# Optimization experiments

Hardware: AMD Instinct MI355X
Metric: run time of the kernel (lower is better)

Reference implementation:

```python
import jax, jax.numpy as jnp
import numpy as np
from jax import lax

B = 64
LATENT = 256
TARGET = LATENT // 2
ACT = 6
HID = 512
DSTATE = 16


def conv2d(x, w, b, stride=2):
    # torch Conv2d(k=4, stride=2, pad=1), w: (O,I,4,4)
    y = lax.conv_general_dilated(x, w, (stride, stride), ((1, 1), (1, 1)),
                                 dimension_numbers=('NCHW', 'OIHW', 'NCHW'))
    return y + b[None, :, None, None]


def deconv2d(x, w, b):
    # torch ConvTranspose2d(k=4, stride=2, pad=1), w: (I,O,4,4)
    w_ = jnp.flip(w, (2, 3)).transpose(1, 0, 2, 3)  # -> OIHW
    y = lax.conv_general_dilated(x, w_, (1, 1), ((2, 2), (2, 2)),
                                 lhs_dilation=(2, 2),
                                 dimension_numbers=('NCHW', 'OIHW', 'NCHW'))
    return y + b[None, :, None, None]


def linear(x, w, b=None):
    y = x @ w.T
    return y if b is None else y + b


def setup_inputs() -> dict:
    key = jax.random.key(0)
    ks = jax.random.split(key, 40)
    s = 0.02
    d = {
        'img_t': jax.random.normal(ks[0], (B, 3, 256, 256), jnp.float32),
        'action_prev': jax.random.normal(ks[1], (B, ACT), jnp.float32),
        'z_prev': jax.random.normal(ks[2], (B, LATENT), jnp.float32),
        'ssm_state_prev': jax.random.normal(ks[3], (B, HID, DSTATE), jnp.float32),
        'eps': jax.random.normal(ks[4], (B, LATENT), jnp.float32),
        # CNN encoder
        'conv1_w': jax.random.normal(ks[5], (32, 3, 4, 4)) * s, 'conv1_b': jnp.zeros(32),
        'conv2_w': jax.random.normal(ks[6], (64, 32, 4, 4)) * s, 'conv2_b': jnp.zeros(64),
        'conv3_w': jax.random.normal(ks[7], (128, 64, 4, 4)) * s, 'conv3_b': jnp.zeros(128),
        'conv4_w': jax.random.normal(ks[8], (256, 128, 4, 4)) * s, 'conv4_b': jnp.zeros(256),
        'enc_fc_w': jax.random.normal(ks[9], (512, 256 * 16 * 16)) * s, 'enc_fc_b': jnp.zeros(512),
        # heads
        'post_w': jax.random.normal(ks[10], (LATENT * 2, 512 + HID)) * s, 'post_b': jnp.zeros(LATENT * 2),
        'prior_w': jax.random.normal(ks[11], (LATENT * 2, HID)) * s, 'prior_b': jnp.zeros(LATENT * 2),
        # ssm input proj
        'ssm_in_w': jax.random.normal(ks[12], (HID, LATENT + ACT)) * s, 'ssm_in_b': jnp.zeros(HID),
        # selective SSM cell
        'A_log': jnp.log(jnp.tile(jnp.arange(1, DSTATE + 1, dtype=jnp.float32), (HID, 1))),
        'B_w': jax.random.normal(ks[13], (DSTATE, HID)) * s,
        'C_w': jax.random.normal(ks[14], (DSTATE, HID)) * s,
        'Delta_w': jax.random.normal(ks[15], (HID, HID)) * s, 'Delta_b': jnp.zeros(HID),
        'D': jnp.ones(HID),
        # mask decoder
        'dec_fc_w': jax.random.normal(ks[16], (128 * 16 * 16, TARGET)) * s, 'dec_fc_b': jnp.zeros(128 * 16 * 16),
        'dc1_w': jax.random.normal(ks[17], (128, 64, 4, 4)) * s, 'dc1_b': jnp.zeros(64),
        'dc2_w': jax.random.normal(ks[18], (64, 32, 4, 4)) * s, 'dc2_b': jnp.zeros(32),
        'dc3_w': jax.random.normal(ks[19], (32, 16, 4, 4)) * s, 'dc3_b': jnp.zeros(16),
        'dc4_w': jax.random.normal(ks[20], (16, 1, 4, 4)) * s, 'dc4_b': jnp.zeros(1),
    }
    return {k: v.astype(jnp.float32) for k, v in d.items()}


def reference(img_t, action_prev, z_prev, ssm_state_prev, eps,
              conv1_w, conv1_b, conv2_w, conv2_b, conv3_w, conv3_b, conv4_w, conv4_b,
              enc_fc_w, enc_fc_b, post_w, post_b, prior_w, prior_b,
              ssm_in_w, ssm_in_b, A_log, B_w, C_w, Delta_w, Delta_b, D,
              dec_fc_w, dec_fc_b, dc1_w, dc1_b, dc2_w, dc2_b, dc3_w, dc3_b, dc4_w, dc4_b):
    # SSM input projection + SiLU
    ssm_in = jax.nn.silu(linear(jnp.concatenate([z_prev, action_prev], -1), ssm_in_w, ssm_in_b))  # (B,HID)
    # Selective SSM cell (single step)
    A = -jnp.exp(A_log)                                   # (HID,DSTATE)
    B_t = linear(ssm_in, B_w)                              # (B,DSTATE)
    C_t = linear(ssm_in, C_w)                              # (B,DSTATE)
    Delta_t = jax.nn.softplus(linear(ssm_in, Delta_w, Delta_b))  # (B,HID)
    A_bar = jnp.exp(Delta_t[:, :, None] * A[None])        # (B,HID,DSTATE)
    Delta_B = Delta_t[:, :, None] * B_t[:, None, :]
    ssm_state_t = A_bar * ssm_state_prev + Delta_B * ssm_in[:, :, None]
    belief = jnp.sum(ssm_state_t * C_t[:, None, :], -1) + D * ssm_in  # (B,HID)
    # Prior
    mu_prior, logvar_prior = jnp.split(linear(belief, prior_w, prior_b), 2, axis=-1)
    # CNN encoder
    h = jax.nn.relu(conv2d(img_t, conv1_w, conv1_b))
    h = jax.nn.relu(conv2d(h, conv2_w, conv2_b))
    h = jax.nn.relu(conv2d(h, conv3_w, conv3_b))
    h = jax.nn.relu(conv2d(h, conv4_w, conv4_b))           # (B,256,16,16)
    cnn_feat = jax.nn.relu(linear(h.reshape(h.shape[0], -1), enc_fc_w, enc_fc_b))  # (B,512)
    # Posterior
    mu_post, logvar_post = jnp.split(linear(jnp.concatenate([cnn_feat, belief], -1), post_w, post_b), 2, axis=-1)
    z_t = mu_post + eps * jnp.exp(0.5 * logvar_post)
    # Mask decoder on target half of latent
    z_target = z_t[:, :TARGET]
    x = linear(z_target, dec_fc_w, dec_fc_b).reshape(-1, 128, 16, 16)
    x = jax.nn.relu(deconv2d(x, dc1_w, dc1_b))
    x = jax.nn.relu(deconv2d(x, dc2_w, dc2_b))
    x = jax.nn.relu(deconv2d(x, dc3_w, dc3_b))
    pred_mask_logits = deconv2d(x, dc4_w, dc4_b)           # (B,1,256,256)
    return (pred_mask_logits, z_t, ssm_state_t, mu_prior, logvar_prior, mu_post, logvar_post)
```

## Files before the change

kernel.cpp:

```cpp
#include <hip/hip_runtime.h>
#include <math.h>

#define BB 64
#define LATENT 256
#define ACTD 6
#define HIDD 512
#define DST 16

typedef __attribute__((ext_vector_type(8))) short bf16x8;
typedef __attribute__((ext_vector_type(4))) float f32x4;

static __device__ __forceinline__ ushort f2bf(float f) {
  unsigned u = __builtin_bit_cast(unsigned, f);
  unsigned r = (u + 0x7FFFu + ((u >> 16) & 1u)) >> 16;
  return (ushort)r;
}
static __device__ __forceinline__ float bf2f(ushort u) {
  return __builtin_bit_cast(float, ((unsigned)u) << 16);
}

#define O_PRED   0
#define O_ZT     4194304
#define O_STATE  4210688
#define O_MUP    4734976
#define O_LVP    4751360
#define O_MUPO   4767744
#define O_LVPO   4784128

#define W_BELIEF 67584u
#define W_CNN    100352u
#define W_ZB16   133120u
#define PW_C2    137216u
#define PW_C3    153600u
#define PW_C4    219136u
#define PW_D1    481280u
#define PW_D2    546816u
#define PW_D3    563200u
#define PW_C1    567296u
#define W_TIMG   602112u
#define W_H1B    13185024u
#define W_H2B    29962240u
#define W_H3B    38350848u
#define W_H4B    42545152u
#define W_SIWT   44642304u
#define W_DWT    44776448u
#define W_PRWT   45038592u
#define W_POWT   45300736u
#define W_ENCP   602112u
#define W_DECO   8990720u
#define W_D1O    10039296u
#define W_D2O    13185024u
#define W_D3O    17379328u

#define ENC_KS 128


static __device__ __forceinline__ void pack_conv_elem(const float* __restrict__ w,
                                                      ushort* __restrict__ o,
                                                      int Cout, int Cin, int id) {
  int NCH = Cin / 2;
  int per = NCH * 512;
  int mt = id / per, r = id % per;
  int kcg = r >> 9, s = r & 511;
  int kg = s >> 7, m = (s >> 3) & 15, k8 = s & 7;
  int co = mt * 16 + m;
  int k = kcg * 32 + kg * 8 + k8;
  int tap = k / Cin, ci = k % Cin;
  o[id] = f2bf(w[(size_t)(co * Cin + ci) * 16 + tap]);
}

static __device__ __forceinline__ void pack_deconv_elem(const float* __restrict__ w,
                                                        ushort* __restrict__ o,
                                                        int Cout, int Cin, int id) {
  int NCH = Cin / 8;
  int perM = NCH * 512;
  int perC = (Cout / 16) * perM;
  int cls = id / perC, r = id % perC;
  int mt = r / perM, r2 = r % perM;
  int kcg = r2 >> 9, s = r2 & 511;
  int kg = s >> 7, m = (s >> 3) & 15, k8 = s & 7;
  int co = mt * 16 + m;
  int k = kcg * 32 + kg * 8 + k8;
  int t = k / Cin, ci = k % Cin;
  int p = (cls >> 1) + 2 * (t >> 1);
  int q = (cls & 1) + 2 * (t & 1);
  o[id] = f2bf(w[(size_t)(ci * Cout + co) * 16 + p * 4 + q]);
}

static __device__ __forceinline__ void pack_conv1_elem(const float* __restrict__ w,
                                                       ushort* __restrict__ o, int id) {
  int mt = id >> 10, r = id & 1023;
  int kcg = r >> 9, s = r & 511;
  int kg = s >> 7, m = (s >> 3) & 15, k8 = s & 7;
  int co = mt * 16 + m;
  int k = kcg * 32 + kg * 8 + k8;
  int tap = k >> 2, ci = k & 3;
  o[id] = (ci < 3) ? f2bf(w[(size_t)(co * 3 + ci) * 16 + tap]) : (ushort)0;
}

__global__ __launch_bounds__(256) void k_pack_all(
    const float* __restrict__ c2w, const float* __restrict__ c3w,
    const float* __restrict__ c4w, const float* __restrict__ d1w,
    const float* __restrict__ d2w, const float* __restrict__ d3w,
    const float* __restrict__ c1w,
    const float* __restrict__ siw, const float* __restrict__ Dw,
    const float* __restrict__ prw, const float* __restrict__ pw,
    ushort* __restrict__ pc2, ushort* __restrict__ pc3, ushort* __restrict__ pc4,
    ushort* __restrict__ pd1, ushort* __restrict__ pd2, ushort* __restrict__ pd3,
    ushort* __restrict__ pc1,
    float* __restrict__ siwT, float* __restrict__ DwT,
    float* __restrict__ prwT, float* __restrict__ powT) {
  int id = blockIdx.x * 256 + threadIdx.x;
  if (id < 32768)            pack_conv_elem(c2w, pc2, 64, 32, id);
  else if (id < 163840)      pack_conv_elem(c3w, pc3, 128, 64, id - 32768);
  else if (id < 688128)      pack_conv_elem(c4w, pc4, 256, 128, id - 163840);
  else if (id < 819200)      pack_deconv_elem(d1w, pd1, 64, 128, id - 688128);
  else if (id < 851968)      pack_deconv_elem(d2w, pd2, 32, 64, id - 819200);
  else if (id < 860160)      pack_deconv_elem(d3w, pd3, 16, 32, id - 851968);
  else if (id < 862208)      pack_conv1_elem(c1w, pc1, id - 860160);
  else if (id < 996352) {
    int r = id - 862208; int k = r >> 9, h = r & 511;
    siwT[r] = siw[(size_t)h * (LATENT + ACTD) + k];
  } else if (id < 1258496) {
    int r = id - 996352; int k = r >> 9, h = r & 511;
    DwT[r] = Dw[(size_t)h * HIDD + k];
  } else if (id < 1520640) {
    int r = id - 1258496; int k = r >> 9, h = r & 511;
    prwT[r] = prw[(size_t)h * HIDD + k];
  } else if (id < 2044928) {
    int r = id - 1520640; int k = r >> 9, j = r & 511;
    powT[r] = pw[(size_t)j * 1024 + k];
  }
}

__global__ __launch_bounds__(512) void k_ssm_timg(
    const float* __restrict__ z_prev, const float* __restrict__ act,
    const float* __restrict__ siwT, const float* __restrict__ sib,
    const float* __restrict__ DwT, const float* __restrict__ Db,
    const float* __restrict__ Bw, const float* __restrict__ Cw,
    const float* __restrict__ Alog, const float* __restrict__ Dv,
    const float* __restrict__ st_prev, float* __restrict__ state_out,
    float* __restrict__ belief_out, const float* __restrict__ prwT,
    const float* __restrict__ prb, float* __restrict__ out,
    const float* __restrict__ img, ushort* __restrict__ timg4) {
  __shared__ float sm[12480];
  int blk = blockIdx.x;
  int tid = threadIdx.x;

  if (blk < 64) {
    float* zs   = sm;
    float* as_  = sm + 256;
    float* si   = sm + 264;
    float* bel  = sm + 776;
    float* part = sm + 1288;
    float* btct = sm + 1416;
    int b = blk;
    int h = tid;
    if (h < 256) zs[h] = z_prev[(size_t)b * LATENT + h];
    if (h >= 256 && h < 256 + ACTD) as_[h - 256] = act[(size_t)b * ACTD + (h - 256)];
    __syncthreads();
    {
      float acc = sib[h];
      #pragma unroll 8
      for (int k = 0; k < LATENT; ++k) acc += zs[k] * siwT[(size_t)k * 512 + h];
      #pragma unroll
      for (int k = 0; k < ACTD; ++k) acc += as_[k] * siwT[(size_t)(LATENT + k) * 512 + h];
      si[h] = acc / (1.f + expf(-acc));
    }
    __syncthreads();
    float d;
    {
      float acc = Db[h];
      #pragma unroll 8
      for (int k = 0; k < HIDD; ++k) acc += si[k] * DwT[(size_t)k * 512 + h];
      d = fmaxf(acc, 0.f) + log1pf(expf(-fabsf(acc)));
    }
    if (h < 128) {
      int half = h >> 6;
      int l = h & 63;
      int n = l & 15, p = l >> 4;
      const float* wr = (half ? Cw : Bw) + (size_t)n * HIDD + p * 128;
      const float* sr = si + p * 128;
      float acc = 0.f;
      #pragma unroll 4
      for (int k = 0; k < 128; k += 4) {
        float4 w4 = *(const float4*)(wr + k);
        acc += sr[k] * w4.x + sr[k+1] * w4.y + sr[k+2] * w4.z + sr[k+3] * w4.w;
      }
      part[(half * 16 + n) * 4 + p] = acc;
    }
    __syncthreads();
    if (h < 32) {
      int half = h >> 4, n = h & 15;
      const float* pp = part + (half * 16 + n) * 4;
      btct[half * 16 + n] = pp[0] + pp[1] + pp[2] + pp[3];
    }
    __syncthreads();
    {
      float si_h = si[h];
      float belv = Dv[h] * si_h;
      const float* al = Alog + (size_t)h * DST;
      const float* sp = st_prev + ((size_t)b * 512 + h) * DST;
      float* so = state_out + ((size_t)b * 512 + h) * DST;
      #pragma unroll
      for (int n = 0; n < DST; ++n) {
        float A = -expf(al[n]);
        float st = expf(d * A) * sp[n] + d * btct[n] * si_h;
        so[n] = st;
        belv += st * btct[16 + n];
      }
      bel[h] = belv;
      belief_out[(size_t)b * 512 + h] = belv;
    }
    __syncthreads();
    {
      float acc = prb[h];
      #pragma unroll 8
      for (int k = 0; k < HIDD; ++k) acc += bel[k] * prwT[(size_t)k * 512 + h];
      if (h < 256) out[O_MUP + b * 256 + h] = acc;
      else         out[O_LVP + b * 256 + (h - 256)] = acc;
    }
  } else {
    float (*ts)[64][65] = (float (*)[64][65])sm;
    int p0 = (blk - 64) << 6;
    #pragma unroll
    for (int c = 0; c < 3; ++c) {
      #pragma unroll
      for (int i = 0; i < 8; ++i) {
        int idx = tid + i * 512;
        int b = idx >> 6, pr = idx & 63;
        ts[c][pr][b] = img[((size_t)b * 3 + c) * 65536 + p0 + pr];
      }
    }
    __syncthreads();
    #pragma unroll
    for (int i = 0; i < 8; ++i) {
      int idx = tid + i * 512;
      int pr = idx >> 6, b = idx & 63;
      uint2 pk;
      pk.x = (unsigned)f2bf(ts[0][pr][b]) | ((unsigned)f2bf(ts[1][pr][b]) << 16);
      pk.y = (unsigned)f2bf(ts[2][pr][b]);
      *(uint2*)(timg4 + ((size_t)(p0 + pr) * 64 + b) * 4) = pk;
    }
  }
}

__global__ __launch_bounds__(256) void k_conv1_mfma(const ushort* __restrict__ in,
                                                    const ushort* __restrict__ wp,
                                                    const float* __restrict__ bias,
                                                    ushort* __restrict__ out) {
  int wid = __builtin_amdgcn_readfirstlane(blockIdx.x * 4 + (threadIdx.x >> 6));
  int lane = threadIdx.x & 63;
  int ox = wid & 127, oy = wid >> 7;
  int ml = lane & 15, khi = lane >> 4;
  f32x4 zero = {0.f, 0.f, 0.f, 0.f};
  f32x4 acc[2][4];
  #pragma unroll
  for (int mt = 0; mt < 2; ++mt)
    #pragma unroll
    for (int nt = 0; nt < 4; ++nt) acc[mt][nt] = zero;
  int by = 2 * oy - 1, bx = 2 * ox - 1;
  bool interior = (oy >= 1) & (oy <= 126) & (ox >= 1) & (ox <= 126);

  #pragma unroll
  for (int kc = 0; kc < 2; ++kc) {
    bf16x8 a0 = *(const bf16x8*)(wp + kc * 512 + lane * 8);
    bf16x8 a1 = *(const bf16x8*)(wp + 1024 + kc * 512 + lane * 8);
    int t0 = kc * 8 + khi * 2;
    int ky0 = t0 >> 2, kx0 = t0 & 3;
    int ky1 = (t0 + 1) >> 2, kx1 = (t0 + 1) & 3;
    int iy0 = by + ky0, ix0 = bx + kx0;
    int iy1 = by + ky1, ix1 = bx + kx1;
    const ushort* pA = in + ((size_t)(iy0 * 256 + ix0) * 64 + ml) * 4;
    const ushort* pB = in + ((size_t)(iy1 * 256 + ix1) * 64 + ml) * 4;
    if (interior) {
      #pragma unroll
      for (int nt = 0; nt < 4; ++nt) {
        uint2 lo = *(const uint2*)(pA + nt * 64);
        uint2 hi = *(const uint2*)(pB + nt * 64);
        uint4 u; u.x = lo.x; u.y = lo.y; u.z = hi.x; u.w = hi.y;
        bf16x8 bb = __builtin_bit_cast(bf16x8, u);
        acc[0][nt] = __builtin_amdgcn_mfma_f32_16x16x32_bf16(a0, bb, acc[0][nt], 0, 0, 0);
        acc[1][nt] = __builtin_amdgcn_mfma_f32_16x16x32_bf16(a1, bb, acc[1][nt], 0, 0, 0);
      }
    } else {
      bool ok0 = ((unsigned)iy0 < 256u) & ((unsigned)ix0 < 256u);
      bool ok1 = ((unsigned)iy1 < 256u) & ((unsigned)ix1 < 256u);
      #pragma unroll
      for (int nt = 0; nt < 4; ++nt) {
        uint2 z2; z2.x = 0u; z2.y = 0u;
        uint2 lo = ok0 ? *(const uint2*)(pA + nt * 64) : z2;
        uint2 hi = ok1 ? *(const uint2*)(pB + nt * 64) : z2;
        uint4 u; u.x = lo.x; u.y = lo.y; u.z = hi.x; u.w = hi.y;
        bf16x8 bb = __builtin_bit_cast(bf16x8, u);
        acc[0][nt] = __builtin_amdgcn_mfma_f32_16x16x32_bf16(a0, bb, acc[0][nt], 0, 0, 0);
        acc[1][nt] = __builtin_amdgcn_mfma_f32_16x16x32_bf16(a1, bb, acc[1][nt], 0, 0, 0);
      }
    }
  }
  int px = oy * 128 + ox;
  int rb = khi * 4;
  #pragma unroll
  for (int mt = 0; mt < 2; ++mt) {
    int co = mt * 16 + rb;
    f32x4 bv = *(const f32x4*)(bias + co);
    #pragma unroll
    for (int nt = 0; nt < 4; ++nt) {
      float v0 = fmaxf(acc[mt][nt][0] + bv[0], 0.f);
      float v1 = fmaxf(acc[mt][nt][1] + bv[1], 0.f);
      float v2 = fmaxf(acc[mt][nt][2] + bv[2], 0.f);
      float v3 = fmaxf(acc[mt][nt][3] + bv[3], 0.f);
      uint2 pk;
      pk.x = (unsigned)f2bf(v0) | ((unsigned)f2bf(v1) << 16);
      pk.y = (unsigned)f2bf(v2) | ((unsigned)f2bf(v3) << 16);
      size_t off = (size_t)px * 2048 + nt * 512 + ((co >> 3) & 3) * 128 + ml * 8 + (co & 7);
      *(uint2*)(out + off) = pk;
    }
  }
}

template<int CIN, int COUT, int MT>
__global__ __launch_bounds__(256) void mfma_conv(const ushort* __restrict__ in,
                                                 const ushort* __restrict__ wp,
                                                 const float* __restrict__ bias,
                                                 ushort* __restrict__ out,
                                                 int Hin, int Win, int Hout, int Wout) {
  constexpr int NMG = COUT / (16 * MT);
  constexpr int NKC = CIN / 32;
  constexpr int NCH = 16 * NKC;
  int wid = __builtin_amdgcn_readfirstlane(blockIdx.x * 4 + (threadIdx.x >> 6));
  int lane = threadIdx.x & 63;
  int mg = wid % NMG;
  int px = wid / NMG;
  int ox = px % Wout, oy = px / Wout;
  if (oy >= Hout) return;
  int mtile0 = mg * MT;
  f32x4 zero = {0.f, 0.f, 0.f, 0.f};
  f32x4 acc[MT][4];
  #pragma unroll
  for (int mt = 0; mt < MT; ++mt)
    #pragma unroll
    for (int nt = 0; nt < 4; ++nt) acc[mt][nt] = zero;
  const ushort* wbase = wp + (size_t)mtile0 * NCH * 512 + lane * 8;
  const size_t mstride = (size_t)NCH * 512;
  bool interior = (oy >= 1) & (oy < Hout - 1) & (ox >= 1) & (ox < Wout - 1);

  if (interior) {
    #pragma unroll
    for (int ky = 0; ky < 4; ++ky) {
      int iy = 2 * oy - 1 + ky;
      #pragma unroll
      for (int kx = 0; kx < 4; ++kx) {
        int ix = 2 * ox - 1 + kx;
        const ushort* ib = in + (size_t)(iy * Win + ix) * (CIN * 64) + lane * 8;
        int tap = ky * 4 + kx;
        #pragma unroll
        for (int kc = 0; kc < NKC; ++kc) {
          int kcg = tap * NKC + kc;
          bf16x8 a[MT], bb[4];
          #pragma unroll
          for (int mt = 0; mt < MT; ++mt)
            a[mt] = *(const bf16x8*)(wbase + mt * mstride + (size_t)kcg * 512);
          #pragma unroll
          for (int nt = 0; nt < 4; ++nt)
            bb[nt] = *(const bf16x8*)(ib + kc * 2048 + nt * 512);
          #pragma unroll
          for (int mt = 0; mt < MT; ++mt)
            #pragma unroll
            for (int nt = 0; nt < 4; ++nt)
              acc[mt][nt] = __builtin_amdgcn_mfma_f32_16x16x32_bf16(a[mt], bb[nt], acc[mt][nt], 0, 0, 0);
        }
      }
    }
  } else {
    for (int ky = 0; ky < 4; ++ky) {
      int iy = 2 * oy - 1 + ky;
      if ((unsigned)iy >= (unsigned)Hin) continue;
      for (int kx = 0; kx < 4; ++kx) {
        int ix = 2 * ox - 1 + kx;
        if ((unsigned)ix >= (unsigned)Win) continue;
        const ushort* ib = in + (size_t)(iy * Win + ix) * (CIN * 64) + lane * 8;
        int tap = ky * 4 + kx;
        #pragma unroll
        for (int kc = 0; kc < NKC; ++kc) {
          int kcg = tap * NKC + kc;
          bf16x8 a[MT], bb[4];
          #pragma unroll
          for (int mt = 0; mt < MT; ++mt)
            a[mt] = *(const bf16x8*)(wbase + mt * mstride + (size_t)kcg * 512);
          #pragma unroll
          for (int nt = 0; nt < 4; ++nt)
            bb[nt] = *(const bf16x8*)(ib + kc * 2048 + nt * 512);
          #pragma unroll
          for (int mt = 0; mt < MT; ++mt)
            #pragma unroll
            for (int nt = 0; nt < 4; ++nt)
              acc[mt][nt] = __builtin_amdgcn_mfma_f32_16x16x32_bf16(a[mt], bb[nt], acc[mt][nt], 0, 0, 0);
        }
      }
    }
  }
  int ml = lane & 15, rb = (lane >> 4) * 4;
  #pragma unroll
  for (int mt = 0; mt < MT; ++mt) {
    int co = mtile0 * 16 + mt * 16 + rb;
    f32x4 bv = *(const f32x4*)(bias + co);
    #pragma unroll
    for (int nt = 0; nt < 4; ++nt) {
      float v0 = fmaxf(acc[mt][nt][0] + bv[0], 0.f);
      float v1 = fmaxf(acc[mt][nt][1] + bv[1], 0.f);
      float v2 = fmaxf(acc[mt][nt][2] + bv[2], 0.f);
      float v3 = fmaxf(acc[mt][nt][3] + bv[3], 0.f);
      uint2 pk;
      pk.x = (unsigned)f2bf(v0) | ((unsigned)f2bf(v1) << 16);
      pk.y = (unsigned)f2bf(v2) | ((unsigned)f2bf(v3) << 16);
      size_t off = (size_t)px * (COUT * 64) + (size_t)(co >> 5) * 2048 + nt * 512
                 + ((co >> 3) & 3) * 128 + ml * 8 + (co & 7);
      *(uint2*)(out + off) = pk;
    }
  }
}

template<int CIN, int COUT, int MT, bool RELU>
__global__ __launch_bounds__(256) void mfma_deconv(const ushort* __restrict__ in,
                                                   const ushort* __restrict__ wp,
                                                   const float* __restrict__ bias,
                                                   ushort* __restrict__ out,
                                                   int Hin, int Win, int Hout, int Wout) {
  constexpr int NMG = COUT / (16 * MT);
  constexpr int NKC = CIN / 32;
  constexpr int NCH = 4 * NKC;
  constexpr int NTS = (COUT >= 32) ? 512 : (COUT * 16);
  int wid = __builtin_amdgcn_readfirstlane(blockIdx.x * 4 + (threadIdx.x >> 6));
  int lane = threadIdx.x & 63;
  int mg = wid % NMG; int r1 = wid / NMG;
  int wo2 = Wout >> 1;
  int pc = (Hout >> 1) * wo2;
  int pxc = r1 % pc; int cls = r1 / pc;
  if (cls >= 4) return;
  int p0 = cls >> 1, q0 = cls & 1;
  int tx = pxc % wo2, ty = pxc / wo2;
  int oy = 2 * ty + 1 - p0, ox = 2 * tx + 1 - q0;
  int iy0 = (oy + 1 - p0) >> 1, ix0 = (ox + 1 - q0) >> 1;
  int mtile0 = mg * MT;
  f32x4 zero = {0.f, 0.f, 0.f, 0.f};
  f32x4 acc[MT][4];
  #pragma unroll
  for (int mt = 0; mt < MT; ++mt)
    #pragma unroll
    for (int nt = 0; nt < 4; ++nt) acc[mt][nt] = zero;
  const ushort* wbase = wp + ((size_t)cls * (COUT / 16) + mtile0) * NCH * 512 + lane * 8;
  const size_t mstride = (size_t)NCH * 512;
  bool interior = (iy0 >= 1) & (iy0 <= Hin - 1) & (ix0 >= 1) & (ix0 <= Win - 1);

  if (interior) {
    #pragma unroll
    for (int i = 0; i < 2; ++i) {
      int iy = iy0 - i;
      #pragma unroll
      for (int j = 0; j < 2; ++j) {
        int ix = ix0 - j;
        const ushort* ib = in + (size_t)(iy * Win + ix) * (CIN * 64) + lane * 8;
        int tap = i * 2 + j;
        #pragma unroll
        for (int kc = 0; kc < NKC; ++kc) {
          int kcg = tap * NKC + kc;
          bf16x8 a[MT], bb[4];
          #pragma unroll
          for (int mt = 0; mt < MT; ++mt)
            a[mt] = *(const bf16x8*)(wbase + mt * mstride + (size_t)kcg * 512);
          #pragma unroll
          for (int nt = 0; nt < 4; ++nt)
            bb[nt] = *(const bf16x8*)(ib + kc * 2048 + nt * 512);
          #pragma unroll
          for (int mt = 0; mt < MT; ++mt)
            #pragma unroll
            for (int nt = 0; nt < 4; ++nt)
              acc[mt][nt] = __builtin_amdgcn_mfma_f32_16x16x32_bf16(a[mt], bb[nt], acc[mt][nt], 0, 0, 0);
        }
      }
    }
  } else {
    for (int i = 0; i < 2; ++i) {
      int iy = iy0 - i;
      if ((unsigned)iy >= (unsigned)Hin) continue;
      for (int j = 0; j < 2; ++j) {
        int ix = ix0 - j;
        if ((unsigned)ix >= (unsigned)Win) continue;
        const ushort* ib = in + (size_t)(iy * Win + ix) * (CIN * 64) + lane * 8;
        int tap = i * 2 + j;
        #pragma unroll
        for (int kc = 0; kc < NKC; ++kc) {
          int kcg = tap * NKC + kc;
          bf16x8 a[MT], bb[4];
          #pragma unroll
          for (int mt = 0; mt < MT; ++mt)
            a[mt] = *(const bf16x8*)(wbase + mt * mstride + (size_t)kcg * 512);
          #pragma unroll
          for (int nt = 0; nt < 4; ++nt)
            bb[nt] = *(const bf16x8*)(ib + kc * 2048 + nt * 512);
          #pragma unroll
          for (int mt = 0; mt < MT; ++mt)
            #pragma unroll
            for (int nt = 0; nt < 4; ++nt)
              acc[mt][nt] = __builtin_amdgcn_mfma_f32_16x16x32_bf16(a[mt], bb[nt], acc[mt][nt], 0, 0, 0);
        }
      }
    }
  }
  int ml = lane & 15, rb = (lane >> 4) * 4;
  int px = oy * Wout + ox;
  #pragma unroll
  for (int mt = 0; mt < MT; ++mt) {
    int co = mtile0 * 16 + mt * 16 + rb;
    f32x4 bv = *(const f32x4*)(bias + co);
    #pragma unroll
    for (int nt = 0; nt < 4; ++nt) {
      float v0 = acc[mt][nt][0] + bv[0];
      float v1 = acc[mt][nt][1] + bv[1];
      float v2 = acc[mt][nt][2] + bv[2];
      float v3 = acc[mt][nt][3] + bv[3];
      if (RELU) { v0=fmaxf(v0,0.f); v1=fmaxf(v1,0.f); v2=fmaxf(v2,0.f); v3=fmaxf(v3,0.f); }
      uint2 pk;
      pk.x = (unsigned)f2bf(v0) | ((unsigned)f2bf(v1) << 16);
      pk.y = (unsigned)f2bf(v2) | ((unsigned)f2bf(v3) << 16);
      size_t off = (size_t)px * (COUT * 64) + (size_t)(co >> 5) * 2048 + (size_t)nt * NTS
                 + ((co >> 3) & 3) * 128 + ml * 8 + (co & 7);
      *(uint2*)(out + off) = pk;
    }
  }
}

#define APXS 1032
__global__ __launch_bounds__(256) void k_encfc_fused(const ushort* __restrict__ h4,
                                                     const float* __restrict__ wE,
                                                     float* __restrict__ partial) {
  __shared__ float smem[8320];
  ushort* au = (ushort*)smem;
  int s = blockIdx.x;
  int bid = (s & 7) * 256 + (s >> 3);
  int mg = bid & 15;
  int ccf = (bid >> 4) & 7;
  int pxg = bid >> 7;
  int tid = threadIdx.x;
  int co0 = mg * 32;
  #pragma unroll
  for (int i = 0; i < 16; ++i) {
    int idx = tid + i * 256;
    int px4 = idx & 3;
    int ci_l = (idx >> 2) & 31;
    int co_l = idx >> 7;
    float4 v = *(const float4*)&wE[((size_t)(co0 + co_l) << 16)
                                   + (size_t)(ccf * 32 + ci_l) * 256 + pxg * 16 + px4 * 4];
    int mt = co_l >> 4, m = co_l & 15;
    int kg = ci_l >> 3, k8 = ci_l & 7;
    int base = mt * 512 + kg * 128 + m * 8 + k8;
    au[(px4 * 4 + 0) * APXS + base] = f2bf(v.x);
    au[(px4 * 4 + 1) * APXS + base] = f2bf(v.y);
    au[(px4 * 4 + 2) * APXS + base] = f2bf(v.z);
    au[(px4 * 4 + 3) * APXS + base] = f2bf(v.w);
  }
  __syncthreads();
  int lane = tid & 63, wv = tid >> 6;
  int ml = lane & 15, rb = (lane >> 4) * 4;
  f32x4 zero = {0.f, 0.f, 0.f, 0.f};
  f32x4 acc[2][4];
  #pragma unroll
  for (int mt = 0; mt < 2; ++mt)
    #pragma unroll
    for (int nt = 0; nt < 4; ++nt) acc[mt][nt] = zero;
  #pragma unroll
  for (int jj = 0; jj < 4; ++jj) {
    int j = wv * 4 + jj;
    int px = pxg * 16 + j;
    bf16x8 a0 = *(const bf16x8*)(au + j * APXS + lane * 8);
    bf16x8 a1 = *(const bf16x8*)(au + j * APXS + 512 + lane * 8);
    const ushort* hb = h4 + (size_t)px * 16384 + ccf * 2048 + lane * 8;
    bf16x8 bb[4];
    #pragma unroll
    for (int nt = 0; nt < 4; ++nt)
      bb[nt] = *(const bf16x8*)(hb + nt * 512);
    #pragma unroll
    for (int nt = 0; nt < 4; ++nt) {
      acc[0][nt] = __builtin_amdgcn_mfma_f32_16x16x32_bf16(a0, bb[nt], acc[0][nt], 0, 0, 0);
      acc[1][nt] = __builtin_amdgcn_mfma_f32_16x16x32_bf16(a1, bb[nt], acc[1][nt], 0, 0, 0);
    }
  }
  __syncthreads();
  #pragma unroll
  for (int mt = 0; mt < 2; ++mt)
    #pragma unroll
    for (int nt = 0; nt < 4; ++nt)
      #pragma unroll
      for (int r = 0; r < 4; ++r)
        smem[wv * 2080 + (mt * 16 + rb + r) * 65 + nt * 16 + ml] = acc[mt][nt][r];
  __syncthreads();
  int ks = pxg * 8 + ccf;
  #pragma unroll
  for (int i = 0; i < 8; ++i) {
    int e = tid + i * 256;
    int b = e & 63, co_l = e >> 6;
    float sum = smem[co_l * 65 + b] + smem[2080 + co_l * 65 + b]
              + smem[4160 + co_l * 65 + b] + smem[6240 + co_l * 65 + b];
    partial[((size_t)(co0 + co_l) * ENC_KS + ks) * 64 + b] = sum;
  }
}

__global__ void k_encfc_red(const float* __restrict__ partial, const float* __restrict__ bias,
                            float* __restrict__ cnn) {
  int id = blockIdx.x * blockDim.x + threadIdx.x;
  int o = id >> 6, b = id & 63;
  float acc = bias[o];
  #pragma unroll 8
  for (int s = 0; s < ENC_KS; ++s) acc += partial[((size_t)o * ENC_KS + s) * 64 + b];
  cnn[(size_t)b * 512 + o] = fmaxf(acc, 0.f);
}

__global__ __launch_bounds__(512) void k_postz(const float* __restrict__ cnn,
                                               const float* __restrict__ belief,
                                               const float* __restrict__ powT,
                                               const float* __restrict__ bias,
                                               const float* __restrict__ eps,
                                               float* __restrict__ out,
                                               ushort* __restrict__ zb) {
  __shared__ float cs[512];
  __shared__ float bs[512];
  __shared__ float sm[512];
  int b = blockIdx.x;
  int j = threadIdx.x;
  cs[j] = cnn[(size_t)b * HIDD + j];
  bs[j] = belief[(size_t)b * HIDD + j];
  __syncthreads();
  float acc = bias[j];
  #pragma unroll 8
  for (int k = 0; k < HIDD; ++k) acc += cs[k] * powT[(size_t)k * 512 + j];
  #pragma unroll 8
  for (int k = 0; k < HIDD; ++k) acc += bs[k] * powT[(size_t)(512 + k) * 512 + j];
  sm[j] = acc;
  if (j < 256) out[O_MUPO + b * 256 + j] = acc;
  else         out[O_LVPO + b * 256 + (j - 256)] = acc;
  __syncthreads();
  if (j < 256) {
    float z = sm[j] + eps[b * 256 + j] * expf(0.5f * sm[j + 256]);
    out[O_ZT + b * 256 + j] = z;
    if (j < 128) zb[b * 128 + j] = f2bf(z);
  }
}

__global__ __launch_bounds__(256) void k_decfc_mfma(const ushort* __restrict__ zb,
                                                    const float* __restrict__ dfw,
                                                    const float* __restrict__ dfb,
                                                    ushort* __restrict__ dec) {
  int wid = __builtin_amdgcn_readfirstlane(blockIdx.x * 4 + (threadIdx.x >> 6));
  int lane = threadIdx.x & 63;
  int m0 = wid * 32;
  int ml = lane & 15, kl = (lane >> 4) * 8;
  f32x4 zero = {0.f, 0.f, 0.f, 0.f};
  f32x4 acc[2][4];
  #pragma unroll
  for (int mt = 0; mt < 2; ++mt)
    #pragma unroll
    for (int nt = 0; nt < 4; ++nt) acc[mt][nt] = zero;
  #pragma unroll
  for (int kc = 0; kc < 4; ++kc) {
    bf16x8 a[2], bb[4];
    #pragma unroll
    for (int mt = 0; mt < 2; ++mt) {
      int m_r = m0 + mt * 16 + ml;
      const float* wr = dfw + (size_t)((m_r & 127) * 256 + (m_r >> 7)) * 128 + kc * 32 + kl;
      float4 u0 = *(const float4*)wr;
      float4 u1 = *(const float4*)(wr + 4);
      bf16x8 av;
      av[0] = (short)f2bf(u0.x); av[1] = (short)f2bf(u0.y);
      av[2] = (short)f2bf(u0.z); av[3] = (short)f2bf(u0.w);
      av[4] = (short)f2bf(u1.x); av[5] = (short)f2bf(u1.y);
      av[6] = (short)f2bf(u1.z); av[7] = (short)f2bf(u1.w);
      a[mt] = av;
    }
    #pragma unroll
    for (int nt = 0; nt < 4; ++nt)
      bb[nt] = *(const bf16x8*)(zb + (size_t)(nt * 16 + ml) * 128 + kc * 32 + kl);
    #pragma unroll
    for (int mt = 0; mt < 2; ++mt)
      #pragma unroll
      for (int nt = 0; nt < 4; ++nt)
        acc[mt][nt] = __builtin_amdgcn_mfma_f32_16x16x32_bf16(a[mt], bb[nt], acc[mt][nt], 0, 0, 0);
  }
  int rb = (lane >> 4) * 4;
  #pragma unroll
  for (int mt = 0; mt < 2; ++mt) {
    int m = m0 + mt * 16 + rb;
    int pix = m >> 7, co = m & 127;
    float bv0 = dfb[(size_t)(co + 0) * 256 + pix];
    float bv1 = dfb[(size_t)(co + 1) * 256 + pix];
    float bv2 = dfb[(size_t)(co + 2) * 256 + pix];
    float bv3 = dfb[(size_t)(co + 3) * 256 + pix];
    #pragma unroll
    for (int nt = 0; nt < 4; ++nt) {
      uint2 pk;
      pk.x = (unsigned)f2bf(acc[mt][nt][0] + bv0) | ((unsigned)f2bf(acc[mt][nt][1] + bv1) << 16);
      pk.y = (unsigned)f2bf(acc[mt][nt][2] + bv2) | ((unsigned)f2bf(acc[mt][nt][3] + bv3) << 16);
      size_t off = (size_t)pix * 8192 + (size_t)(co >> 5) * 2048 + nt * 512
                 + ((co >> 3) & 3) * 128 + ml * 8 + (co & 7);
      *(uint2*)(dec + off) = pk;
    }
  }
}

__global__ __launch_bounds__(256) void k_d4t(const ushort* __restrict__ in,
                                             const float* __restrict__ w,
                                             const float* __restrict__ bias,
                                             float* __restrict__ out) {
  __shared__ float lds[64][65];
  int blk = blockIdx.x;
  int oy = blk >> 2, ox0 = (blk & 3) << 6;
  int t = threadIdx.x;
  int b = t & 63, sub = t >> 6;
  float bv = bias[0];
  for (int j = 0; j < 16; ++j) {
    int oxl = j * 4 + sub;
    int ox = ox0 + oxl;
    int p0 = (oy + 1) & 1, q0 = (ox + 1) & 1;
    int iy0 = (oy + 1 - p0) >> 1, ix0 = (ox + 1 - q0) >> 1;
    float acc = bv;
    #pragma unroll
    for (int i = 0; i < 2; ++i) {
      int iy = iy0 - i;
      if ((unsigned)iy >= 128u) continue;
      int p = p0 + 2 * i;
      #pragma unroll
      for (int jj = 0; jj < 2; ++jj) {
        int ix = ix0 - jj;
        if ((unsigned)ix >= 128u) continue;
        int q = q0 + 2 * jj;
        const ushort* base = in + (size_t)(iy * 128 + ix) * 1024 + (b >> 4) * 256 + (b & 15) * 8;
        bf16x8 v0 = *(const bf16x8*)(base);
        bf16x8 v1 = *(const bf16x8*)(base + 128);
        const float* wq = w + p * 4 + q;
        #pragma unroll
        for (int ci = 0; ci < 8; ++ci) acc += bf2f((ushort)v0[ci]) * wq[ci * 16];
        #pragma unroll
        for (int ci = 0; ci < 8; ++ci) acc += bf2f((ushort)v1[ci]) * wq[(ci + 8) * 16];
      }
    }
    lds[oxl][b] = acc;
  }
  __syncthreads();
  #pragma unroll
  for (int j = 0; j < 16; ++j) {
    int idx = t + j * 256;
    int b2 = idx >> 6, oxl = idx & 63;
    out[(size_t)b2 * 65536 + oy * 256 + ox0 + oxl] = lds[oxl][b2];
  }
}


extern "C" void kernel_launch(void* const* d_in, const int* in_sizes, int n_in,
                              void* d_out, int out_size, void* d_ws, size_t ws_size,
                              hipStream_t stream) {
  const float* img      = (const float*)d_in[0];
  const float* act      = (const float*)d_in[1];
  const float* z_prev   = (const float*)d_in[2];
  const float* st_prev  = (const float*)d_in[3];
  const float* eps      = (const float*)d_in[4];
  const float* c1w = (const float*)d_in[5];  const float* c1b = (const float*)d_in[6];
  const float* c2w = (const float*)d_in[7];  const float* c2b = (const float*)d_in[8];
  const float* c3w = (const float*)d_in[9];  const float* c3b = (const float*)d_in[10];
  const float* c4w = (const float*)d_in[11]; const float* c4b = (const float*)d_in[12];
  const float* efw = (const float*)d_in[13]; const float* efb = (const float*)d_in[14];
  const float* pow_ = (const float*)d_in[15]; const float* pob = (const float*)d_in[16];
  const float* prw = (const float*)d_in[17]; const float* prb = (const float*)d_in[18];
  const float* siw = (const float*)d_in[19]; const float* sib = (const float*)d_in[20];
  const float* Alog = (const float*)d_in[21];
  const float* Bw = (const float*)d_in[22];  const float* Cw = (const float*)d_in[23];
  const float* Dw = (const float*)d_in[24];  const float* Db = (const float*)d_in[25];
  const float* Dv = (const float*)d_in[26];
  const float* dfw = (const float*)d_in[27]; const float* dfb = (const float*)d_in[28];
  const float* d1w = (const float*)d_in[29]; const float* d1b = (const float*)d_in[30];
  const float* d2w = (const float*)d_in[31]; const float* d2b = (const float*)d_in[32];
  const float* d3w = (const float*)d_in[33]; const float* d3b = (const float*)d_in[34];
  const float* d4w = (const float*)d_in[35]; const float* d4b = (const float*)d_in[36];

  float* ws = (float*)d_ws;
  float* out = (float*)d_out;

  ushort* pc2 = (ushort*)(ws + PW_C2);
  ushort* pc3 = (ushort*)(ws + PW_C3);
  ushort* pc4 = (ushort*)(ws + PW_C4);
  ushort* pd1 = (ushort*)(ws + PW_D1);
  ushort* pd2 = (ushort*)(ws + PW_D2);
  ushort* pd3 = (ushort*)(ws + PW_D3);
  ushort* pc1 = (ushort*)(ws + PW_C1);
  ushort* timg4 = (ushort*)(ws + W_TIMG);
  ushort* h1b = (ushort*)(ws + W_H1B);
  ushort* h2b = (ushort*)(ws + W_H2B);
  ushort* h3b = (ushort*)(ws + W_H3B);
  ushort* h4b = (ushort*)(ws + W_H4B);
  ushort* deco = (ushort*)(ws + W_DECO);
  ushort* d1o = (ushort*)(ws + W_D1O);
  ushort* d2o = (ushort*)(ws + W_D2O);
  ushort* d3o = (ushort*)(ws + W_D3O);
  ushort* zb = (ushort*)(ws + W_ZB16);
  float* siwT = ws + W_SIWT;
  float* DwT  = ws + W_DWT;
  float* prwT = ws + W_PRWT;
  float* powT = ws + W_POWT;

  k_pack_all<<<7988, 256, 0, stream>>>(c2w, c3w, c4w, d1w, d2w, d3w, c1w,
                                       siw, Dw, prw, pow_,
                                       pc2, pc3, pc4, pd1, pd2, pd3, pc1,
                                       siwT, DwT, prwT, powT);

  k_ssm_timg<<<1088, 512, 0, stream>>>(z_prev, act, siwT, sib, DwT, Db, Bw, Cw,
                                       Alog, Dv, st_prev, out + O_STATE,
                                       ws + W_BELIEF, prwT, prb, out,
                                       img, timg4);

  k_conv1_mfma<<<4096, 256, 0, stream>>>(timg4, pc1, c1b, h1b);
  mfma_conv<32, 64, 4><<<1024, 256, 0, stream>>>(h1b, pc2, c2b, h2b, 128, 128, 64, 64);
  mfma_conv<64, 128, 4><<<512, 256, 0, stream>>>(h2b, pc3, c3b, h3b, 64, 64, 32, 32);
  mfma_conv<128, 256, 2><<<512, 256, 0, stream>>>(h3b, pc4, c4b, h4b, 32, 32, 16, 16);

  k_encfc_fused<<<2048, 256, 0, stream>>>(h4b, efw, ws + W_ENCP);
  k_encfc_red<<<128, 256, 0, stream>>>(ws + W_ENCP, efb, ws + W_CNN);

  k_postz<<<64, 512, 0, stream>>>(ws + W_CNN, ws + W_BELIEF, powT, pob, eps, out, zb);

  k_decfc_mfma<<<256, 256, 0, stream>>>(zb, dfw, dfb, deco);
  mfma_deconv<128, 64, 2, true><<<512, 256, 0, stream>>>(deco, pd1, d1b, d1o, 16, 16, 32, 32);
  mfma_deconv<64, 32, 2, true><<<1024, 256, 0, stream>>>(d1o, pd2, d2b, d2o, 32, 32, 64, 64);
  mfma_deconv<32, 16, 1, true><<<4096, 256, 0, stream>>>(d2o, pd3, d3b, d3o, 64, 64, 128, 128);
  k_d4t<<<1024, 256, 0, stream>>>(d3o, d4w, d4b, out + O_PRED);
}
```

Baseline: 435.4 us.

## Split SSM and posterior matvecs over 1024 threads with pair-interleaved weights

The small per-batch matvec kernels (SSM input projection, dt projection, prior head and posterior head) now use 1024 threads. Two threads split the K dimension for each output and combine their partial sums through shared memory. The transposed weights are repacked so each thread reads a float2 holding two consecutive K values, halving the number of load instructions. The goal is lower latency in these serial, low-parallelism 64-block kernels, at the cost of extra syncs and a reduction step. The image transpose path in the same kernel is adjusted to the larger block size.

```diff
diff --git a/kernel.cpp b/kernel.cpp
--- a/kernel.cpp
+++ b/kernel.cpp
@@ -122,18 +122,21 @@
     int r = id - 862208; int k = r >> 9, h = r & 511;
     siwT[r] = siw[(size_t)h * (LATENT + ACTD) + k];
   } else if (id < 1258496) {
-    int r = id - 996352; int k = r >> 9, h = r & 511;
-    DwT[r] = Dw[(size_t)h * HIDD + k];
+    int r = id - 996352;
+    int p = r >> 10, h2 = (r & 1023) >> 1, e = r & 1;
+    DwT[r] = Dw[(size_t)h2 * HIDD + (2 * p + e)];
   } else if (id < 1520640) {
-    int r = id - 1258496; int k = r >> 9, h = r & 511;
-    prwT[r] = prw[(size_t)h * HIDD + k];
+    int r = id - 1258496;
+    int p = r >> 10, h2 = (r & 1023) >> 1, e = r & 1;
+    prwT[r] = prw[(size_t)h2 * HIDD + (2 * p + e)];
   } else if (id < 2044928) {
-    int r = id - 1520640; int k = r >> 9, j = r & 511;
-    powT[r] = pw[(size_t)j * 1024 + k];
-  }
-}
-
-__global__ __launch_bounds__(512) void k_ssm_timg(
+    int r = id - 1520640;
+    int p = r >> 10, j2 = (r & 1023) >> 1, e = r & 1;
+    powT[r] = pw[(size_t)j2 * 1024 + (2 * p + e)];
+  }
+}
+
+__global__ __launch_bounds__(1024) void k_ssm_timg(
     const float* __restrict__ z_prev, const float* __restrict__ act,
     const float* __restrict__ siwT, const float* __restrict__ sib,
     const float* __restrict__ DwT, const float* __restrict__ Db,
@@ -148,55 +151,71 @@
   int tid = threadIdx.x;
 
   if (blk < 64) {
-    float* zs   = sm;
-    float* as_  = sm + 256;
+    float* xs   = sm;
     float* si   = sm + 264;
     float* bel  = sm + 776;
-    float* part = sm + 1288;
-    float* btct = sm + 1416;
+    float* red  = sm + 1288;
+    float* part = sm + 1800;
+    float* btct = sm + 1928;
     int b = blk;
-    int h = tid;
-    if (h < 256) zs[h] = z_prev[(size_t)b * LATENT + h];
-    if (h >= 256 && h < 256 + ACTD) as_[h - 256] = act[(size_t)b * ACTD + (h - 256)];
+    int h = tid & 511;
+    int half = tid >> 9;
+    if (tid < 256) xs[tid] = z_prev[(size_t)b * LATENT + tid];
+    else if (tid < 256 + ACTD) xs[tid] = act[(size_t)b * ACTD + (tid - 256)];
+    else if (tid < 264) xs[tid] = 0.f;
     __syncthreads();
     {
-      float acc = sib[h];
-      #pragma unroll 8
-      for (int k = 0; k < LATENT; ++k) acc += zs[k] * siwT[(size_t)k * 512 + h];
-      #pragma unroll
-      for (int k = 0; k < ACTD; ++k) acc += as_[k] * siwT[(size_t)(LATENT + k) * 512 + h];
-      si[h] = acc / (1.f + expf(-acc));
+      float acc = half ? 0.f : sib[h];
+      int k0 = half * 131;
+      #pragma unroll 4
+      for (int k = k0; k < k0 + 131; ++k) acc += xs[k] * siwT[(size_t)k * 512 + h];
+      if (half) red[h] = acc;
+      __syncthreads();
+      if (!half) {
+        float t = acc + red[h];
+        si[h] = t / (1.f + expf(-t));
+      }
     }
     __syncthreads();
-    float d;
+    float d = 0.f;
     {
-      float acc = Db[h];
-      #pragma unroll 8
-      for (int k = 0; k < HIDD; ++k) acc += si[k] * DwT[(size_t)k * 512 + h];
-      d = fmaxf(acc, 0.f) + log1pf(expf(-fabsf(acc)));
-    }
-    if (h < 128) {
-      int half = h >> 6;
-      int l = h & 63;
+      float acc = half ? 0.f : Db[h];
+      const float* wb = DwT + (size_t)(half * 128) * 1024 + h * 2;
+      const float* sb = si + half * 256;
+      #pragma unroll 4
+      for (int p = 0; p < 128; ++p) {
+        float2 w2 = *(const float2*)(wb + (size_t)p * 1024);
+        acc += sb[2 * p] * w2.x + sb[2 * p + 1] * w2.y;
+      }
+      if (half) red[h] = acc;
+      __syncthreads();
+      if (!half) {
+        float t = acc + red[h];
+        d = fmaxf(t, 0.f) + log1pf(expf(-fabsf(t)));
+      }
+    }
+    if (tid < 128) {
+      int hf2 = tid >> 6;
+      int l = tid & 63;
       int n = l & 15, p = l >> 4;
-      const float* wr = (half ? Cw : Bw) + (size_t)n * HIDD + p * 128;
+      const float* wr = (hf2 ? Cw : Bw) + (size_t)n * HIDD + p * 128;
       const float* sr = si + p * 128;
-      float acc = 0.f;
+      float a2 = 0.f;
       #pragma unroll 4
       for (int k = 0; k < 128; k += 4) {
         float4 w4 = *(const float4*)(wr + k);
-        acc += sr[k] * w4.x + sr[k+1] * w4.y + sr[k+2] * w4.z + sr[k+3] * w4.w;
-      }
-      part[(half * 16 + n) * 4 + p] = acc;
+        a2 += sr[k] * w4.x + sr[k+1] * w4.y + sr[k+2] * w4.z + sr[k+3] * w4.w;
+      }
+      part[(hf2 * 16 + n) * 4 + p] = a2;
     }
     __syncthreads();
-    if (h < 32) {
-      int half = h >> 4, n = h & 15;
-      const float* pp = part + (half * 16 + n) * 4;
-      btct[half * 16 + n] = pp[0] + pp[1] + pp[2] + pp[3];
+    if (tid < 32) {
+      int hf2 = tid >> 4, n = tid & 15;
+      const float* pp = part + (hf2 * 16 + n) * 4;
+      btct[hf2 * 16 + n] = pp[0] + pp[1] + pp[2] + pp[3];
     }
     __syncthreads();
-    {
+    if (!half) {
       float si_h = si[h];
       float belv = Dv[h] * si_h;
       const float* al = Alog + (size_t)h * DST;
@@ -214,11 +233,21 @@
     }
     __syncthreads();
     {
-      float acc = prb[h];
-      #pragma unroll 8
-      for (int k = 0; k < HIDD; ++k) acc += bel[k] * prwT[(size_t)k * 512 + h];
-      if (h < 256) out[O_MUP + b * 256 + h] = acc;
-      else         out[O_LVP + b * 256 + (h - 256)] = acc;
+      float acc = half ? 0.f : prb[h];
+      const float* wb = prwT + (size_t)(half * 128) * 1024 + h * 2;
+      const float* bb2 = bel + half * 256;
+      #pragma unroll 4
+      for (int p = 0; p < 128; ++p) {
+        float2 w2 = *(const float2*)(wb + (size_t)p * 1024);
+        acc += bb2[2 * p] * w2.x + bb2[2 * p + 1] * w2.y;
+      }
+      if (half) red[h] = acc;
+      __syncthreads();
+      if (!half) {
+        float t = acc + red[h];
+        if (h < 256) out[O_MUP + b * 256 + h] = t;
+        else         out[O_LVP + b * 256 + (h - 256)] = t;
+      }
     }
   } else {
     float (*ts)[64][65] = (float (*)[64][65])sm;
@@ -226,16 +255,16 @@
     #pragma unroll
     for (int c = 0; c < 3; ++c) {
       #pragma unroll
-      for (int i = 0; i < 8; ++i) {
-        int idx = tid + i * 512;
+      for (int i = 0; i < 4; ++i) {
+        int idx = tid + i * 1024;
         int b = idx >> 6, pr = idx & 63;
         ts[c][pr][b] = img[((size_t)b * 3 + c) * 65536 + p0 + pr];
       }
     }
     __syncthreads();
     #pragma unroll
-    for (int i = 0; i < 8; ++i) {
-      int idx = tid + i * 512;
+    for (int i = 0; i < 4; ++i) {
+      int idx = tid + i * 1024;
       int pr = idx >> 6, b = idx & 63;
       uint2 pk;
       pk.x = (unsigned)f2bf(ts[0][pr][b]) | ((unsigned)f2bf(ts[1][pr][b]) << 16);
@@ -616,34 +645,45 @@
   cnn[(size_t)b * 512 + o] = fmaxf(acc, 0.f);
 }
 
-__global__ __launch_bounds__(512) void k_postz(const float* __restrict__ cnn,
-                                               const float* __restrict__ belief,
-                                               const float* __restrict__ powT,
-                                               const float* __restrict__ bias,
-                                               const float* __restrict__ eps,
-                                               float* __restrict__ out,
-                                               ushort* __restrict__ zb) {
+__global__ __launch_bounds__(1024) void k_postz(const float* __restrict__ cnn,
+                                                const float* __restrict__ belief,
+                                                const float* __restrict__ powT,
+                                                const float* __restrict__ bias,
+                                                const float* __restrict__ eps,
+                                                float* __restrict__ out,
+                                                ushort* __restrict__ zb) {
   __shared__ float cs[512];
   __shared__ float bs[512];
-  __shared__ float sm[512];
+  __shared__ float smv[512];
+  __shared__ float red[512];
   int b = blockIdx.x;
-  int j = threadIdx.x;
-  cs[j] = cnn[(size_t)b * HIDD + j];
-  bs[j] = belief[(size_t)b * HIDD + j];
+  int tid = threadIdx.x;
+  int j = tid & 511;
+  int half = tid >> 9;
+  if (tid < 512) cs[tid] = cnn[(size_t)b * HIDD + tid];
+  else           bs[tid - 512] = belief[(size_t)b * HIDD + (tid - 512)];
   __syncthreads();
-  float acc = bias[j];
-  #pragma unroll 8
-  for (int k = 0; k < HIDD; ++k) acc += cs[k] * powT[(size_t)k * 512 + j];
-  #pragma unroll 8
-  for (int k = 0; k < HIDD; ++k) acc += bs[k] * powT[(size_t)(512 + k) * 512 + j];
-  sm[j] = acc;
-  if (j < 256) out[O_MUPO + b * 256 + j] = acc;
-  else         out[O_LVPO + b * 256 + (j - 256)] = acc;
+  float acc = half ? 0.f : bias[j];
+  const float* wb = powT + (size_t)(half * 256) * 1024 + j * 2;
+  const float* src = half ? bs : cs;
+  #pragma unroll 4
+  for (int p = 0; p < 256; ++p) {
+    float2 w2 = *(const float2*)(wb + (size_t)p * 1024);
+    acc += src[2 * p] * w2.x + src[2 * p + 1] * w2.y;
+  }
+  if (half) red[j] = acc;
   __syncthreads();
-  if (j < 256) {
-    float z = sm[j] + eps[b * 256 + j] * expf(0.5f * sm[j + 256]);
-    out[O_ZT + b * 256 + j] = z;
-    if (j < 128) zb[b * 128 + j] = f2bf(z);
+  if (!half) {
+    float t = acc + red[j];
+    smv[j] = t;
+    if (j < 256) out[O_MUPO + b * 256 + j] = t;
+    else         out[O_LVPO + b * 256 + (j - 256)] = t;
+  }
+  __syncthreads();
+  if (tid < 256) {
+    float z = smv[tid] + eps[b * 256 + tid] * expf(0.5f * smv[tid + 256]);
+    out[O_ZT + b * 256 + tid] = z;
+    if (tid < 128) zb[b * 128 + tid] = f2bf(z);
   }
 }
 
@@ -811,10 +851,10 @@
                                        pc2, pc3, pc4, pd1, pd2, pd3, pc1,
                                        siwT, DwT, prwT, powT);
 
-  k_ssm_timg<<<1088, 512, 0, stream>>>(z_prev, act, siwT, sib, DwT, Db, Bw, Cw,
-                                       Alog, Dv, st_prev, out + O_STATE,
-                                       ws + W_BELIEF, prwT, prb, out,
-                                       img, timg4);
+  k_ssm_timg<<<1088, 1024, 0, stream>>>(z_prev, act, siwT, sib, DwT, Db, Bw, Cw,
+                                        Alog, Dv, st_prev, out + O_STATE,
+                                        ws + W_BELIEF, prwT, prb, out,
+                                        img, timg4);
 
   k_conv1_mfma<<<4096, 256, 0, stream>>>(timg4, pc1, c1b, h1b);
   mfma_conv<32, 64, 4><<<1024, 256, 0, stream>>>(h1b, pc2, c2b, h2b, 128, 128, 64, 64);
@@ -824,7 +864,7 @@
   k_encfc_fused<<<2048, 256, 0, stream>>>(h4b, efw, ws + W_ENCP);
   k_encfc_red<<<128, 256, 0, stream>>>(ws + W_ENCP, efb, ws + W_CNN);
 
-  k_postz<<<64, 512, 0, stream>>>(ws + W_CNN, ws + W_BELIEF, powT, pob, eps, out, zb);
+  k_postz<<<64, 1024, 0, stream>>>(ws + W_CNN, ws + W_BELIEF, powT, pob, eps, out, zb);
 
   k_decfc_mfma<<<256, 256, 0, stream>>>(zb, dfw, dfb, deco);
   mfma_deconv<128, 64, 2, true><<<512, 256, 0, stream>>>(deco, pd1, d1b, d1o, 16, 16, 32, 32);
```

Result: faster. 401.1 us (-7.9%).
